# Kernel optimization log

Measured on AMD Instinct MI355X. Metric: run time of the kernel, lower is better.

## Reference

```python
import jax, jax.numpy as jnp
import numpy as np

PRUNE_RATIO = 0.5
NOISE_SCALE = 0.1
MIXUP_ALPHA = 0.05
TEMPERATURE = 0.5
B, N, D = 32, 4096, 256


def setup_inputs() -> dict:
    key = jax.random.key(0)
    k1, k2, k3 = jax.random.split(key, 3)
    seq = jax.random.normal(k1, (B, N, D), dtype=jnp.float32)
    attn_weights = jax.random.uniform(k2, (B, N), dtype=jnp.float32)
    uniform_noise = jax.random.uniform(k3, (B, N), dtype=jnp.float32)
    return {"seq": seq, "attn_weights": attn_weights, "uniform_noise": uniform_noise}


def reference(seq, attn_weights, uniform_noise):
    b, n, d = seq.shape
    k = max(1, int(n * (1.0 - PRUNE_RATIO)))
    # training branch: gumbel noise from the provided uniform draw
    gumbel = -jnp.log(-jnp.log(uniform_noise + 1e-10) + 1e-10)
    noisy = attn_weights + NOISE_SCALE * gumbel                      # (B, N)
    soft = jax.nn.softmax(noisy / TEMPERATURE, axis=-1)              # (B, N)
    _, top_idx = jax.lax.top_k(soft, k)                              # (B, K) int32
    # gather selected tokens: (B, K, D)
    selected = jnp.take_along_axis(seq, top_idx[:, :, None], axis=1)
    # mixup: mean of the pruned (non-selected) tokens
    mask = jnp.ones((b, n), dtype=seq.dtype).at[
        jnp.arange(b)[:, None], top_idx
    ].set(0.0)                                                       # (B, N), 1 on pruned
    remaining_sum = jnp.einsum('bn,bnd->bd', mask, seq)              # (B, D)
    remaining_count = mask.sum(axis=1, keepdims=True) + 1e-10        # (B, 1)
    remaining_mean = remaining_sum / remaining_count                 # (B, D)
    return selected + MIXUP_ALPHA * remaining_mean[:, None, :]       # (B, K, D)
```

## Files before the change

kernel.cpp:

```cpp
#include <hip/hip_runtime.h>

#define B_ 32
#define N_ 4096
#define D_ 256
#define K_ 2048

#define ISPLIT 2
#define JSPLIT 16
#define EPT 8
#define JSLICE (N_ / JSPLIT)

__global__ __launch_bounds__(256) void key_kernel(
    const float* __restrict__ attn, const float* __restrict__ noise,
    unsigned long long* __restrict__ keys,
    unsigned long long* __restrict__ rankBuf64,
    float* __restrict__ meanAccum) {
  const int t = blockIdx.x * 256 + threadIdx.x;
  float u = noise[t];
  float a = attn[t];
  float x = __fadd_rn(u, 1e-10f);
  float l1 = (float)log((double)x);
  float inner = __fadd_rn(-l1, 1e-10f);
  float g = -(float)log((double)inner);
  float noisy = __fadd_rn(a, __fmul_rn(0.1f, g));
  unsigned int fb = __float_as_uint(noisy);
  fb = (fb & 0x80000000u) ? ~fb : (fb | 0x80000000u);
  int i = t & (N_ - 1);
  keys[t] = ((unsigned long long)fb << 32) | (unsigned int)(~i);
  if (t < B_ * N_ / 4) rankBuf64[t] = 0ull;
  if (t < B_ * D_) meanAccum[t] = 0.0f;
}

__global__ __launch_bounds__(256) void rank_kernel(
    const unsigned long long* __restrict__ keys,
    unsigned long long* __restrict__ rankBuf64) {
  const int b = blockIdx.y;
  const int ic = blockIdx.x >> 4;
  const int jc = blockIdx.x & (JSPLIT - 1);
  __shared__ __align__(16) unsigned long long lk[JSLICE];

  const unsigned long long* __restrict__ bk = keys + (size_t)b * N_;

  lk[threadIdx.x] = bk[jc * JSLICE + threadIdx.x];

  const int ibase = ic * (N_ / ISPLIT) + threadIdx.x * EPT;
  unsigned long long ki[EPT];
  const ulonglong2* __restrict__ gi2 = (const ulonglong2*)(bk + ibase);
#pragma unroll
  for (int e2 = 0; e2 < EPT / 2; ++e2) {
    ulonglong2 v = gi2[e2];
    ki[2 * e2] = v.x;
    ki[2 * e2 + 1] = v.y;
  }
  __syncthreads();

  const ulonglong2* lk2 = (const ulonglong2*)lk;
  unsigned int rk[EPT] = {0u, 0u, 0u, 0u, 0u, 0u, 0u, 0u};
#pragma unroll 4
  for (int j = 0; j < JSLICE / 2; ++j) {
    ulonglong2 v = lk2[j];
#pragma unroll
    for (int e = 0; e < EPT; ++e) {
      rk[e] += (v.x > ki[e]);
      rk[e] += (v.y > ki[e]);
    }
  }

  unsigned long long p0 =
      (unsigned long long)rk[0] | ((unsigned long long)rk[1] << 16) |
      ((unsigned long long)rk[2] << 32) | ((unsigned long long)rk[3] << 48);
  unsigned long long p1 =
      (unsigned long long)rk[4] | ((unsigned long long)rk[5] << 16) |
      ((unsigned long long)rk[6] << 32) | ((unsigned long long)rk[7] << 48);
  const size_t q = ((size_t)b * N_ + ibase) >> 2;
  atomicAdd(&rankBuf64[q], p0);
  atomicAdd(&rankBuf64[q + 1], p1);
}

__global__ __launch_bounds__(256) void mean_kernel(
    const unsigned short* __restrict__ rankBuf16, const float* __restrict__ seq,
    float* __restrict__ meanAccum) {
  const int b = blockIdx.y;
  const int ibase = blockIdx.x * 128;
  __shared__ int plist[128];
  __shared__ int pcount;
  if (threadIdx.x == 0) pcount = 0;
  __syncthreads();
  if (threadIdx.x < 128) {
    const int i = ibase + threadIdx.x;
    const unsigned int rank = rankBuf16[(size_t)b * N_ + i];
    if (rank >= K_) {
      int slot = atomicAdd(&pcount, 1);
      plist[slot] = i;
    }
  }
  __syncthreads();
  const int cnt = pcount;

  const int dv = threadIdx.x & 63;
  const int sub = threadIdx.x >> 6;
  float4 acc = make_float4(0.f, 0.f, 0.f, 0.f);
  for (int r = sub; r < cnt; r += 4) {
    const float4* row = (const float4*)(seq + ((size_t)b * N_ + plist[r]) * D_);
    float4 v = row[dv];
    acc.x += v.x; acc.y += v.y; acc.z += v.z; acc.w += v.w;
  }

  __shared__ float4 red[4][64];
  red[sub][dv] = acc;
  __syncthreads();
  if (sub == 0) {
    float4 s0 = red[0][dv], s1 = red[1][dv], s2 = red[2][dv], s3 = red[3][dv];
    float sx = s0.x + s1.x + s2.x + s3.x;
    float sy = s0.y + s1.y + s2.y + s3.y;
    float sz = s0.z + s1.z + s2.z + s3.z;
    float sw = s0.w + s1.w + s2.w + s3.w;
    float* dst = meanAccum + b * D_ + dv * 4;
    atomicAdd(dst + 0, sx);
    atomicAdd(dst + 1, sy);
    atomicAdd(dst + 2, sz);
    atomicAdd(dst + 3, sw);
  }
}

__global__ __launch_bounds__(256) void out_kernel(
    const unsigned short* __restrict__ rankBuf16, const float* __restrict__ seq,
    const float* __restrict__ meanAccum, float* __restrict__ out) {
  const int b = blockIdx.y;
  const int ibase = blockIdx.x * 128;
  __shared__ int pl_i[128];
  __shared__ unsigned short pl_r[128];
  __shared__ int pcount;
  if (threadIdx.x == 0) pcount = 0;
  __syncthreads();
  if (threadIdx.x < 128) {
    const int i = ibase + threadIdx.x;
    const unsigned int rank = rankBuf16[(size_t)b * N_ + i];
    if (rank < K_) {
      int slot = atomicAdd(&pcount, 1);
      pl_i[slot] = i;
      pl_r[slot] = (unsigned short)rank;
    }
  }
  __syncthreads();
  const int cnt = pcount;

  const int dv = threadIdx.x & 63;
  const int sub = threadIdx.x >> 6;
  float4 m = ((const float4*)(meanAccum + b * D_))[dv];
  const float s = 0.05f * (1.0f / 2048.0f);
  float4 mix;
  mix.x = m.x * s; mix.y = m.y * s; mix.z = m.z * s; mix.w = m.w * s;

  for (int r = sub; r < cnt; r += 4) {
    const float4* row = (const float4*)(seq + ((size_t)b * N_ + pl_i[r]) * D_);
    float4 v = row[dv];
    float4 o;
    o.x = v.x + mix.x; o.y = v.y + mix.y; o.z = v.z + mix.z; o.w = v.w + mix.w;
    ((float4*)(out + ((size_t)b * K_ + pl_r[r]) * D_))[dv] = o;
  }
}

extern "C" void kernel_launch(void* const* d_in, const int* in_sizes, int n_in,
                              void* d_out, int out_size, void* d_ws, size_t ws_size,
                              hipStream_t stream) {
  const float* seq  = (const float*)d_in[0];
  const float* attn = (const float*)d_in[1];
  const float* nois = (const float*)d_in[2];
  float* out = (float*)d_out;

  float* meanAccum = (float*)d_ws;
  unsigned long long* keys =
      (unsigned long long*)((char*)d_ws + (size_t)B_ * D_ * 4);
  unsigned long long* rankBuf64 =
      (unsigned long long*)((char*)keys + (size_t)B_ * N_ * 8);
  unsigned short* rankBuf16 = (unsigned short*)rankBuf64;

  key_kernel<<<(B_ * N_) / 256, 256, 0, stream>>>(attn, nois, keys, rankBuf64, meanAccum);
  rank_kernel<<<dim3(ISPLIT * JSPLIT, B_), 256, 0, stream>>>(keys, rankBuf64);
  mean_kernel<<<dim3(32, B_), 256, 0, stream>>>(rankBuf16, seq, meanAccum);
  out_kernel<<<dim3(32, B_), 256, 0, stream>>>(rankBuf16, seq, meanAccum, out);
}
```

Baseline: 261.9 us.

## Select top-k by radix histogram, then rank only the selected keys

The full N×N pairwise ranking is replaced by a per-batch radix-select kernel that uses 8-bit histograms over the key's high word to find the k-th threshold. It breaks ties by pairwise comparison of the low words. Only the K selected keys are compacted and ranked pairwise, which cuts the comparison work by about a factor of four. The mean and output kernels now read a selection flag and the compacted slots. The cost is a serial select kernel with only 32 blocks, plus an extra launch.

```diff
diff --git a/kernel.cpp b/kernel.cpp
--- a/kernel.cpp
+++ b/kernel.cpp
@@ -5,15 +5,14 @@
 #define D_ 256
 #define K_ 2048
 
-#define ISPLIT 2
-#define JSPLIT 16
-#define EPT 8
-#define JSLICE (N_ / JSPLIT)
+#define TJSPLIT 16
+#define TEPT 8
+#define TJSLICE (K_ / TJSPLIT)
 
 __global__ __launch_bounds__(256) void key_kernel(
     const float* __restrict__ attn, const float* __restrict__ noise,
     unsigned long long* __restrict__ keys,
-    unsigned long long* __restrict__ rankBuf64,
+    unsigned long long* __restrict__ rankSlot64,
     float* __restrict__ meanAccum) {
   const int t = blockIdx.x * 256 + threadIdx.x;
   float u = noise[t];
@@ -27,27 +26,118 @@
   fb = (fb & 0x80000000u) ? ~fb : (fb | 0x80000000u);
   int i = t & (N_ - 1);
   keys[t] = ((unsigned long long)fb << 32) | (unsigned int)(~i);
-  if (t < B_ * N_ / 4) rankBuf64[t] = 0ull;
+  if (t < B_ * K_ / 4) rankSlot64[t] = 0ull;
   if (t < B_ * D_) meanAccum[t] = 0.0f;
 }
 
-__global__ __launch_bounds__(256) void rank_kernel(
+__global__ __launch_bounds__(256) void select_kernel(
     const unsigned long long* __restrict__ keys,
-    unsigned long long* __restrict__ rankBuf64) {
+    unsigned long long* __restrict__ topKeys,
+    unsigned char* __restrict__ selFlag) {
+  const int b = blockIdx.x;
+  const int tid = threadIdx.x;
+  const unsigned long long* __restrict__ bk = keys + (size_t)b * N_;
+
+  unsigned long long kreg[16];
+#pragma unroll
+  for (int e = 0; e < 16; ++e) kreg[e] = bk[e * 256 + tid];
+
+  __shared__ unsigned int hist[256];
+  __shared__ unsigned int sParam[2];
+  __shared__ unsigned int tieLo[N_];
+  __shared__ unsigned int tieCnt;
+  __shared__ unsigned int topCnt;
+
+  unsigned int selMask = 0u;
+  unsigned int actMask = 0xFFFFu;
+  unsigned int budget = K_;
+
+  if (tid == 0) topCnt = 0u;
+
+  for (int p = 0; p < 4; ++p) {
+    const int shift = 24 - 8 * p;
+    hist[tid] = 0u;
+    if (tid == 0) tieCnt = 0u;
+    __syncthreads();
+#pragma unroll
+    for (int e = 0; e < 16; ++e) {
+      if (actMask & (1u << e)) {
+        unsigned int h = (unsigned int)(kreg[e] >> 32);
+        atomicAdd(&hist[(h >> shift) & 255u], 1u);
+      }
+    }
+    __syncthreads();
+    {
+      unsigned int sv = 0u;
+      for (int u = tid; u < 256; ++u) sv += hist[u];
+      unsigned int svn = sv - hist[tid];
+      if (sv >= budget && svn < budget) {
+        sParam[0] = (unsigned int)tid;
+        sParam[1] = svn;
+      }
+    }
+    __syncthreads();
+    const unsigned int t = sParam[0];
+    const unsigned int A = sParam[1];
+    budget -= A;
+#pragma unroll
+    for (int e = 0; e < 16; ++e) {
+      if (actMask & (1u << e)) {
+        unsigned int byteV = ((unsigned int)(kreg[e] >> 32) >> shift) & 255u;
+        if (byteV > t) { selMask |= (1u << e); actMask &= ~(1u << e); }
+        else if (byteV < t) { actMask &= ~(1u << e); }
+      }
+    }
+    __syncthreads();
+  }
+
+#pragma unroll
+  for (int e = 0; e < 16; ++e) {
+    if (actMask & (1u << e)) {
+      unsigned int slot = atomicAdd(&tieCnt, 1u);
+      tieLo[slot] = (unsigned int)kreg[e];
+    }
+  }
+  __syncthreads();
+  const unsigned int E = tieCnt;
+  const unsigned int R = budget;
+#pragma unroll
+  for (int e = 0; e < 16; ++e) {
+    if (actMask & (1u << e)) {
+      unsigned int lo = (unsigned int)kreg[e];
+      unsigned int c = 0u;
+      for (unsigned int k2 = 0u; k2 < E; ++k2) c += (tieLo[k2] > lo);
+      if (c < R) selMask |= (1u << e);
+    }
+  }
+
+#pragma unroll
+  for (int e = 0; e < 16; ++e) {
+    const int idx = e * 256 + tid;
+    const unsigned int sel = (selMask >> e) & 1u;
+    selFlag[(size_t)b * N_ + idx] = (unsigned char)sel;
+    if (sel) {
+      unsigned int slot = atomicAdd(&topCnt, 1u);
+      topKeys[(size_t)b * K_ + slot] = kreg[e];
+    }
+  }
+}
+
+__global__ __launch_bounds__(256) void rank_top_kernel(
+    const unsigned long long* __restrict__ topKeys,
+    unsigned long long* __restrict__ rankSlot64) {
   const int b = blockIdx.y;
-  const int ic = blockIdx.x >> 4;
-  const int jc = blockIdx.x & (JSPLIT - 1);
-  __shared__ __align__(16) unsigned long long lk[JSLICE];
-
-  const unsigned long long* __restrict__ bk = keys + (size_t)b * N_;
-
-  lk[threadIdx.x] = bk[jc * JSLICE + threadIdx.x];
-
-  const int ibase = ic * (N_ / ISPLIT) + threadIdx.x * EPT;
-  unsigned long long ki[EPT];
+  const int jc = blockIdx.x;
+  __shared__ __align__(16) unsigned long long lk[TJSLICE];
+
+  const unsigned long long* __restrict__ bk = topKeys + (size_t)b * K_;
+  if (threadIdx.x < TJSLICE) lk[threadIdx.x] = bk[jc * TJSLICE + threadIdx.x];
+
+  const int ibase = threadIdx.x * TEPT;
+  unsigned long long ki[TEPT];
   const ulonglong2* __restrict__ gi2 = (const ulonglong2*)(bk + ibase);
 #pragma unroll
-  for (int e2 = 0; e2 < EPT / 2; ++e2) {
+  for (int e2 = 0; e2 < TEPT / 2; ++e2) {
     ulonglong2 v = gi2[e2];
     ki[2 * e2] = v.x;
     ki[2 * e2 + 1] = v.y;
@@ -55,12 +145,12 @@
   __syncthreads();
 
   const ulonglong2* lk2 = (const ulonglong2*)lk;
-  unsigned int rk[EPT] = {0u, 0u, 0u, 0u, 0u, 0u, 0u, 0u};
+  unsigned int rk[TEPT] = {0u, 0u, 0u, 0u, 0u, 0u, 0u, 0u};
 #pragma unroll 4
-  for (int j = 0; j < JSLICE / 2; ++j) {
+  for (int j = 0; j < TJSLICE / 2; ++j) {
     ulonglong2 v = lk2[j];
 #pragma unroll
-    for (int e = 0; e < EPT; ++e) {
+    for (int e = 0; e < TEPT; ++e) {
       rk[e] += (v.x > ki[e]);
       rk[e] += (v.y > ki[e]);
     }
@@ -72,13 +162,13 @@
   unsigned long long p1 =
       (unsigned long long)rk[4] | ((unsigned long long)rk[5] << 16) |
       ((unsigned long long)rk[6] << 32) | ((unsigned long long)rk[7] << 48);
-  const size_t q = ((size_t)b * N_ + ibase) >> 2;
-  atomicAdd(&rankBuf64[q], p0);
-  atomicAdd(&rankBuf64[q + 1], p1);
+  const size_t q = ((size_t)b * K_ + ibase) >> 2;
+  atomicAdd(&rankSlot64[q], p0);
+  atomicAdd(&rankSlot64[q + 1], p1);
 }
 
 __global__ __launch_bounds__(256) void mean_kernel(
-    const unsigned short* __restrict__ rankBuf16, const float* __restrict__ seq,
+    const unsigned char* __restrict__ selFlag, const float* __restrict__ seq,
     float* __restrict__ meanAccum) {
   const int b = blockIdx.y;
   const int ibase = blockIdx.x * 128;
@@ -88,8 +178,7 @@
   __syncthreads();
   if (threadIdx.x < 128) {
     const int i = ibase + threadIdx.x;
-    const unsigned int rank = rankBuf16[(size_t)b * N_ + i];
-    if (rank >= K_) {
+    if (selFlag[(size_t)b * N_ + i] == 0) {
       int slot = atomicAdd(&pcount, 1);
       plist[slot] = i;
     }
@@ -124,40 +213,30 @@
 }
 
 __global__ __launch_bounds__(256) void out_kernel(
-    const unsigned short* __restrict__ rankBuf16, const float* __restrict__ seq,
+    const unsigned long long* __restrict__ topKeys,
+    const unsigned short* __restrict__ rankSlot16,
+    const float* __restrict__ seq,
     const float* __restrict__ meanAccum, float* __restrict__ out) {
   const int b = blockIdx.y;
-  const int ibase = blockIdx.x * 128;
-  __shared__ int pl_i[128];
-  __shared__ unsigned short pl_r[128];
-  __shared__ int pcount;
-  if (threadIdx.x == 0) pcount = 0;
-  __syncthreads();
-  if (threadIdx.x < 128) {
-    const int i = ibase + threadIdx.x;
-    const unsigned int rank = rankBuf16[(size_t)b * N_ + i];
-    if (rank < K_) {
-      int slot = atomicAdd(&pcount, 1);
-      pl_i[slot] = i;
-      pl_r[slot] = (unsigned short)rank;
-    }
-  }
-  __syncthreads();
-  const int cnt = pcount;
-
+  const int sbase = blockIdx.x * 128;
   const int dv = threadIdx.x & 63;
   const int sub = threadIdx.x >> 6;
+
   float4 m = ((const float4*)(meanAccum + b * D_))[dv];
   const float s = 0.05f * (1.0f / 2048.0f);
   float4 mix;
   mix.x = m.x * s; mix.y = m.y * s; mix.z = m.z * s; mix.w = m.w * s;
 
-  for (int r = sub; r < cnt; r += 4) {
-    const float4* row = (const float4*)(seq + ((size_t)b * N_ + pl_i[r]) * D_);
+  for (int r = sub; r < 128; r += 4) {
+    const int slot = sbase + r;
+    unsigned long long key = topKeys[(size_t)b * K_ + slot];
+    const int i = (int)(~(unsigned int)key) & (N_ - 1);
+    const unsigned int rank = rankSlot16[(size_t)b * K_ + slot];
+    const float4* row = (const float4*)(seq + ((size_t)b * N_ + i) * D_);
     float4 v = row[dv];
     float4 o;
     o.x = v.x + mix.x; o.y = v.y + mix.y; o.z = v.z + mix.z; o.w = v.w + mix.w;
-    ((float4*)(out + ((size_t)b * K_ + pl_r[r]) * D_))[dv] = o;
+    ((float4*)(out + ((size_t)b * K_ + rank) * D_))[dv] = o;
   }
 }
 
@@ -172,12 +251,17 @@
   float* meanAccum = (float*)d_ws;
   unsigned long long* keys =
       (unsigned long long*)((char*)d_ws + (size_t)B_ * D_ * 4);
-  unsigned long long* rankBuf64 =
+  unsigned long long* topKeys =
       (unsigned long long*)((char*)keys + (size_t)B_ * N_ * 8);
-  unsigned short* rankBuf16 = (unsigned short*)rankBuf64;
-
-  key_kernel<<<(B_ * N_) / 256, 256, 0, stream>>>(attn, nois, keys, rankBuf64, meanAccum);
-  rank_kernel<<<dim3(ISPLIT * JSPLIT, B_), 256, 0, stream>>>(keys, rankBuf64);
-  mean_kernel<<<dim3(32, B_), 256, 0, stream>>>(rankBuf16, seq, meanAccum);
-  out_kernel<<<dim3(32, B_), 256, 0, stream>>>(rankBuf16, seq, meanAccum, out);
-}
+  unsigned long long* rankSlot64 =
+      (unsigned long long*)((char*)topKeys + (size_t)B_ * K_ * 8);
+  unsigned short* rankSlot16 = (unsigned short*)rankSlot64;
+  unsigned char* selFlag =
+      (unsigned char*)((char*)rankSlot64 + (size_t)B_ * K_ * 2);
+
+  key_kernel<<<(B_ * N_) / 256, 256, 0, stream>>>(attn, nois, keys, rankSlot64, meanAccum);
+  select_kernel<<<B_, 256, 0, stream>>>(keys, topKeys, selFlag);
+  rank_top_kernel<<<dim3(TJSPLIT, B_), 256, 0, stream>>>(topKeys, rankSlot64);
+  mean_kernel<<<dim3(32, B_), 256, 0, stream>>>(selFlag, seq, meanAccum);
+  out_kernel<<<dim3(16, B_), 256, 0, stream>>>(topKeys, rankSlot16, seq, meanAccum, out);
+}
```

After: 271.3 us. +3.6%, slower.
